# Optimization experiments

Hardware: AMD Instinct MI355X
Metric: run time of the kernel (lower is better)

Reference implementation:

```python
import jax, jax.numpy as jnp
import numpy as np

N_SUBKEYS = 256
D_KEY = 128
D_MODEL = 1024
TOP_K = 8


def setup_inputs() -> dict:
    key = jax.random.key(0)
    ks = jax.random.split(key, 7)
    B, T = 4, 2048
    x = jax.random.normal(ks[0], (B, T, D_MODEL), dtype=jnp.float32)
    keys_a = jax.random.normal(ks[1], (N_SUBKEYS, D_KEY), dtype=jnp.float32) * 0.02
    keys_b = jax.random.normal(ks[2], (N_SUBKEYS, D_KEY), dtype=jnp.float32) * 0.02
    values = jax.random.normal(ks[3], (N_SUBKEYS * N_SUBKEYS, D_MODEL), dtype=jnp.float32) * 0.01
    # nn.Linear(d_model, 2*d_key, bias=False): weight shape [2*d_key, d_model]
    Wq = jax.random.normal(ks[4], (2 * D_KEY, D_MODEL), dtype=jnp.float32) * (1.0 / np.sqrt(D_MODEL))
    gate_w = jax.random.normal(ks[5], (1, D_MODEL), dtype=jnp.float32) * (1.0 / np.sqrt(D_MODEL))
    gate_b = jnp.full((1,), -2.0, dtype=jnp.float32)
    return {"x": x, "keys_a": keys_a, "keys_b": keys_b, "values": values,
            "Wq": Wq, "gate_w": gate_w, "gate_b": gate_b}


def reference(x, keys_a, keys_b, values, Wq, gate_w, gate_b):
    B, T, D = x.shape
    tk = TOP_K
    q = jnp.einsum('btd,kd->btk', x, Wq)          # [B,T,2*d_key]
    qa, qb = jnp.split(q, 2, axis=-1)
    scores_a = jnp.einsum('btd,nd->btn', qa, keys_a)  # [B,T,n_subkeys]
    scores_b = jnp.einsum('btd,nd->btn', qb, keys_b)
    va, ia = jax.lax.top_k(scores_a, tk)          # [B,T,tk]
    vb, ib = jax.lax.top_k(scores_b, tk)
    # Cartesian combination of sub-key candidates -> tk*tk flat candidates
    flat_idx = (ia[..., :, None] * N_SUBKEYS + ib[..., None, :]).reshape(B, T, tk * tk)
    combined = (va[..., :, None] + vb[..., None, :]).reshape(B, T, tk * tk)
    fv, fi = jax.lax.top_k(combined, tk)          # [B,T,tk]
    final_idx = jnp.take_along_axis(flat_idx, fi, axis=-1)  # [B,T,tk]
    weights = jax.nn.softmax(fv, axis=-1)
    vals = values[final_idx]                      # [B,T,tk,D] gather from big table
    mem_out = jnp.einsum('btk,btkd->btd', weights, vals)
    g = jax.nn.sigmoid(jnp.einsum('btd,od->bto', x, gate_w) + gate_b)  # [B,T,1]
    return x + g * mem_out
```

## Files before the change

kernel.cpp:

```cpp
#include <hip/hip_runtime.h>
#include <math.h>

#define D_MODEL 1024
#define D_KEY 128
#define NSUB 256
#define NTOK 8192

typedef __attribute__((ext_vector_type(8))) short bf16x8;
typedef __attribute__((ext_vector_type(4))) float f32x4;

__device__ __forceinline__ unsigned short f2bf(float f) {
  union { float f; unsigned int u; } v; v.f = f;
  return (unsigned short)((v.u + 0x7fffu + ((v.u >> 16) & 1u)) >> 16);
}
__device__ __forceinline__ float bf2f(unsigned short u) {
  union { unsigned int u; float f; } v; v.u = ((unsigned int)u) << 16;
  return v.f;
}

__global__ __launch_bounds__(256) void k_prep(const float* __restrict__ Wq,
                                              const float* __restrict__ keys_a,
                                              const float* __restrict__ keys_b,
                                              unsigned short* __restrict__ Mt) {
  __shared__ float ks[4][128];
  const int tid = threadIdx.x;
  const int c0 = blockIdx.x * 4;
  const float* kk = (c0 < 256) ? keys_a : keys_b;
  const int rbase = c0 & 255;
  const int joff = (c0 < 256) ? 0 : 128;
  if (tid < 128) {
    const int r = tid >> 5, f = tid & 31;
    *(float4*)&ks[r][f * 4] = *(const float4*)&kk[(size_t)(rbase + r) * 128 + f * 4];
  }
  __syncthreads();
  const int d0 = tid * 4;
  float acc[4][4] = {};
  for (int j = 0; j < 128; j++) {
    const float4 wv = *(const float4*)&Wq[(size_t)(joff + j) * D_MODEL + d0];
#pragma unroll
    for (int r = 0; r < 4; r++) {
      const float kj = ks[r][j];
      acc[r][0] += wv.x * kj; acc[r][1] += wv.y * kj;
      acc[r][2] += wv.z * kj; acc[r][3] += wv.w * kj;
    }
  }
#pragma unroll
  for (int r = 0; r < 4; r++) {
    ushort4 o;
    o.x = f2bf(acc[r][0]); o.y = f2bf(acc[r][1]);
    o.z = f2bf(acc[r][2]); o.w = f2bf(acc[r][3]);
    *(ushort4*)&Mt[(size_t)(c0 + r) * D_MODEL + d0] = o;
  }
}

__global__ __launch_bounds__(256) void k_scores(const float* __restrict__ x,
                                                const unsigned short* __restrict__ Mt,
                                                unsigned short* __restrict__ scores) {
  __shared__ __align__(16) short Asd[64 * 32];
  __shared__ __align__(16) short Bsd[128 * 32];
  const int tid = threadIdx.x;
  const int t0 = blockIdx.y * 64;
  const int c0 = blockIdx.x * 128;
  const int arow = tid >> 2, aseg = tid & 3;
  const int brow = tid >> 1, bhalf = tid & 1;
  const float* xp = x + (size_t)(t0 + arow) * D_MODEL + aseg * 8;
  const unsigned short* mp = Mt + (size_t)(c0 + brow) * D_MODEL + bhalf * 16;
  const int l = tid & 63, w = tid >> 6;
  const int rw0 = (w & 1) * 32;
  const int cw0 = (w >> 1) * 64;
  const int fr = l & 15, q = l >> 4;

  f32x4 acc[2][4];
#pragma unroll
  for (int mi = 0; mi < 2; mi++)
#pragma unroll
    for (int ni = 0; ni < 4; ni++) acc[mi][ni] = (f32x4){0.f, 0.f, 0.f, 0.f};

  for (int kc = 0; kc < D_MODEL; kc += 32) {
    const float4 a0 = *(const float4*)(xp + kc);
    const float4 a1 = *(const float4*)(xp + kc + 4);
    bf16x8 pk;
    pk[0] = (short)f2bf(a0.x); pk[1] = (short)f2bf(a0.y);
    pk[2] = (short)f2bf(a0.z); pk[3] = (short)f2bf(a0.w);
    pk[4] = (short)f2bf(a1.x); pk[5] = (short)f2bf(a1.y);
    pk[6] = (short)f2bf(a1.z); pk[7] = (short)f2bf(a1.w);
    *(bf16x8*)&Asd[arow * 32 + aseg * 8] = pk;
    const uint4 b0 = *(const uint4*)(mp + kc);
    const uint4 b1 = *(const uint4*)(mp + kc + 8);
    *(uint4*)&Bsd[brow * 32 + bhalf * 16] = b0;
    *(uint4*)&Bsd[brow * 32 + bhalf * 16 + 8] = b1;
    __syncthreads();
    bf16x8 af[2], bfr[4];
#pragma unroll
    for (int mi = 0; mi < 2; mi++)
      af[mi] = *(const bf16x8*)&Asd[(rw0 + mi * 16 + fr) * 32 + q * 8];
#pragma unroll
    for (int ni = 0; ni < 4; ni++)
      bfr[ni] = *(const bf16x8*)&Bsd[(cw0 + ni * 16 + fr) * 32 + q * 8];
#pragma unroll
    for (int mi = 0; mi < 2; mi++)
#pragma unroll
      for (int ni = 0; ni < 4; ni++)
        acc[mi][ni] = __builtin_amdgcn_mfma_f32_16x16x32_bf16(af[mi], bfr[ni], acc[mi][ni], 0, 0, 0);
    __syncthreads();
  }
#pragma unroll
  for (int mi = 0; mi < 2; mi++)
#pragma unroll
    for (int ni = 0; ni < 4; ni++)
#pragma unroll
      for (int r = 0; r < 4; r++) {
        const int row = t0 + rw0 + mi * 16 + q * 4 + r;
        const int col = c0 + cw0 + ni * 16 + fr;
        scores[(size_t)row * 512 + col] = f2bf(acc[mi][ni][r]);
      }
}

__global__ __launch_bounds__(256) void k_topk(const float* __restrict__ x,
                                              const float* __restrict__ values,
                                              const float* __restrict__ gate_w,
                                              const float* __restrict__ gate_b,
                                              const unsigned short* __restrict__ scores,
                                              float* __restrict__ out) {
  const int tid = threadIdx.x;
  const int lane = tid & 63;
  const int wave = tid >> 6;
  const size_t t = (size_t)blockIdx.x * 4 + wave;

  const unsigned short* srow = scores + t * 512;
  const ushort4 ra = *(const ushort4*)&srow[lane * 4];
  const ushort4 rb = *(const ushort4*)&srow[256 + lane * 4];
  float sva[4] = {bf2f(ra.x), bf2f(ra.y), bf2f(ra.z), bf2f(ra.w)};
  float svb[4] = {bf2f(rb.x), bf2f(rb.y), bf2f(rb.z), bf2f(rb.w)};

  float tav[8], tbv[8];
  int tai[8], tbi[8];
#pragma unroll
  for (int sel = 0; sel < 8; sel++) {
    float bv = sva[0]; int bi = lane * 4;
#pragma unroll
    for (int c = 1; c < 4; c++)
      if (sva[c] > bv) { bv = sva[c]; bi = lane * 4 + c; }
#pragma unroll
    for (int off = 32; off >= 1; off >>= 1) {
      const float ov = __shfl_xor(bv, off);
      const int oi = __shfl_xor(bi, off);
      if (ov > bv || (ov == bv && oi < bi)) { bv = ov; bi = oi; }
    }
    tav[sel] = bv; tai[sel] = bi;
    if ((bi >> 2) == lane) sva[bi & 3] = -INFINITY;
  }
#pragma unroll
  for (int sel = 0; sel < 8; sel++) {
    float bv = svb[0]; int bi = lane * 4;
#pragma unroll
    for (int c = 1; c < 4; c++)
      if (svb[c] > bv) { bv = svb[c]; bi = lane * 4 + c; }
#pragma unroll
    for (int off = 32; off >= 1; off >>= 1) {
      const float ov = __shfl_xor(bv, off);
      const int oi = __shfl_xor(bi, off);
      if (ov > bv || (ov == bv && oi < bi)) { bv = ov; bi = oi; }
    }
    tbv[sel] = bv; tbi[sel] = bi;
    if ((bi >> 2) == lane) svb[bi & 3] = -INFINITY;
  }
  float cv = tav[lane >> 3] + tbv[lane & 7];
  float fv[8]; int fidx[8];
#pragma unroll
  for (int sel = 0; sel < 8; sel++) {
    float bv = cv; int bi = lane;
#pragma unroll
    for (int off = 32; off >= 1; off >>= 1) {
      const float ov = __shfl_xor(bv, off);
      const int oi = __shfl_xor(bi, off);
      if (ov > bv || (ov == bv && oi < bi)) { bv = ov; bi = oi; }
    }
    fv[sel] = bv;
    fidx[sel] = tai[bi >> 3] * NSUB + tbi[bi & 7];
    if (lane == bi) cv = -INFINITY;
  }
  float wgt[8];
  {
    float s = 0.f;
#pragma unroll
    for (int k = 0; k < 8; k++) { wgt[k] = __expf(fv[k] - fv[0]); s += wgt[k]; }
    const float inv = 1.0f / s;
#pragma unroll
    for (int k = 0; k < 8; k++) wgt[k] *= inv;
  }

  const size_t base = t * D_MODEL + lane * 16;
  float4 xv[4], gw[4];
#pragma unroll
  for (int u = 0; u < 4; u++) {
    xv[u] = *(const float4*)&x[base + u * 4];
    gw[u] = *(const float4*)&gate_w[lane * 16 + u * 4];
  }
  float gp = 0.f;
#pragma unroll
  for (int u = 0; u < 4; u++)
    gp += xv[u].x * gw[u].x + xv[u].y * gw[u].y + xv[u].z * gw[u].z + xv[u].w * gw[u].w;
#pragma unroll
  for (int off = 32; off >= 1; off >>= 1) gp += __shfl_xor(gp, off);
  const float g = 1.0f / (1.0f + __expf(-(gp + gate_b[0])));

  float4 facc[4] = {{0, 0, 0, 0}, {0, 0, 0, 0}, {0, 0, 0, 0}, {0, 0, 0, 0}};
#pragma unroll
  for (int k = 0; k < 8; k++) {
    const float wk = wgt[k];
    const float* vrow = values + (size_t)fidx[k] * D_MODEL + lane * 16;
#pragma unroll
    for (int u = 0; u < 4; u++) {
      const float4 v4 = *(const float4*)&vrow[u * 4];
      facc[u].x += wk * v4.x; facc[u].y += wk * v4.y;
      facc[u].z += wk * v4.z; facc[u].w += wk * v4.w;
    }
  }
#pragma unroll
  for (int u = 0; u < 4; u++) {
    float4 o;
    o.x = xv[u].x + g * facc[u].x; o.y = xv[u].y + g * facc[u].y;
    o.z = xv[u].z + g * facc[u].z; o.w = xv[u].w + g * facc[u].w;
    *(float4*)&out[base + u * 4] = o;
  }
}

extern "C" void kernel_launch(void* const* d_in, const int* in_sizes, int n_in,
                              void* d_out, int out_size, void* d_ws, size_t ws_size,
                              hipStream_t stream) {
  const float* x = (const float*)d_in[0];
  const float* keys_a = (const float*)d_in[1];
  const float* keys_b = (const float*)d_in[2];
  const float* values = (const float*)d_in[3];
  const float* Wq = (const float*)d_in[4];
  const float* gate_w = (const float*)d_in[5];
  const float* gate_b = (const float*)d_in[6];
  float* out = (float*)d_out;

  unsigned short* scores = (unsigned short*)d_ws;
  unsigned short* Mt = (unsigned short*)((char*)d_ws + (size_t)NTOK * 512 * 2);

  k_prep<<<128, 256, 0, stream>>>(Wq, keys_a, keys_b, Mt);
  k_scores<<<dim3(4, 128), 256, 0, stream>>>(x, Mt, scores);
  k_topk<<<NTOK / 4, 256, 0, stream>>>(x, values, gate_w, gate_b, scores, out);
}
```

Baseline: 515.2 us.

## Split top-k selection and value gather into separate kernels

The fused top-k plus gather kernel is split in two. A selection kernel writes the softmax weights and flat indices per token to workspace. A separate gather kernel then uses one 256-thread block per token, each thread loading one float4 per value row, with the gate dot product reduced across waves through shared memory. The aim is more parallelism and memory-level concurrency for the random gather of value rows, at the cost of an extra launch and a small round trip of indices and weights through global memory.

After: 464.1 us. 9.9% less time.

```diff
diff --git a/kernel.cpp b/kernel.cpp
--- a/kernel.cpp
+++ b/kernel.cpp
@@ -116,12 +116,9 @@
       }
 }
 
-__global__ __launch_bounds__(256) void k_topk(const float* __restrict__ x,
-                                              const float* __restrict__ values,
-                                              const float* __restrict__ gate_w,
-                                              const float* __restrict__ gate_b,
-                                              const unsigned short* __restrict__ scores,
-                                              float* __restrict__ out) {
+__global__ __launch_bounds__(256) void k_topk_sel(const unsigned short* __restrict__ scores,
+                                                  float* __restrict__ wout,
+                                                  int* __restrict__ iout) {
   const int tid = threadIdx.x;
   const int lane = tid & 63;
   const int wave = tid >> 6;
@@ -181,49 +178,60 @@
     if (lane == bi) cv = -INFINITY;
   }
   float wgt[8];
-  {
-    float s = 0.f;
-#pragma unroll
-    for (int k = 0; k < 8; k++) { wgt[k] = __expf(fv[k] - fv[0]); s += wgt[k]; }
-    const float inv = 1.0f / s;
-#pragma unroll
-    for (int k = 0; k < 8; k++) wgt[k] *= inv;
-  }
-
-  const size_t base = t * D_MODEL + lane * 16;
-  float4 xv[4], gw[4];
-#pragma unroll
-  for (int u = 0; u < 4; u++) {
-    xv[u] = *(const float4*)&x[base + u * 4];
-    gw[u] = *(const float4*)&gate_w[lane * 16 + u * 4];
-  }
-  float gp = 0.f;
-#pragma unroll
-  for (int u = 0; u < 4; u++)
-    gp += xv[u].x * gw[u].x + xv[u].y * gw[u].y + xv[u].z * gw[u].z + xv[u].w * gw[u].w;
+  float s = 0.f;
+#pragma unroll
+  for (int k = 0; k < 8; k++) { wgt[k] = __expf(fv[k] - fv[0]); s += wgt[k]; }
+  const float inv = 1.0f / s;
+#pragma unroll
+  for (int k = 0; k < 8; k++) wgt[k] *= inv;
+
+  if (lane == 0) {
+    *(float4*)&wout[t * 8] = make_float4(wgt[0], wgt[1], wgt[2], wgt[3]);
+    *(float4*)&wout[t * 8 + 4] = make_float4(wgt[4], wgt[5], wgt[6], wgt[7]);
+    *(int4*)&iout[t * 8] = make_int4(fidx[0], fidx[1], fidx[2], fidx[3]);
+    *(int4*)&iout[t * 8 + 4] = make_int4(fidx[4], fidx[5], fidx[6], fidx[7]);
+  }
+}
+
+__global__ __launch_bounds__(256) void k_gather(const float* __restrict__ x,
+                                                const float* __restrict__ values,
+                                                const float* __restrict__ gate_w,
+                                                const float* __restrict__ gate_b,
+                                                const float* __restrict__ win,
+                                                const int* __restrict__ iin,
+                                                float* __restrict__ out) {
+  __shared__ float swgt[8];
+  __shared__ int sidx[8];
+  __shared__ float gpart[4];
+  const int tid = threadIdx.x;
+  const int lane = tid & 63;
+  const int wave = tid >> 6;
+  const size_t t = blockIdx.x;
+
+  if (tid < 2) *(float4*)&swgt[tid * 4] = *(const float4*)&win[t * 8 + tid * 4];
+  else if (tid < 4) *(int4*)&sidx[(tid - 2) * 4] = *(const int4*)&iin[t * 8 + (tid - 2) * 4];
+
+  const float4 x4 = *(const float4*)&x[t * D_MODEL + tid * 4];
+  const float4 gw4 = *(const float4*)&gate_w[tid * 4];
+  float gp = x4.x * gw4.x + x4.y * gw4.y + x4.z * gw4.z + x4.w * gw4.w;
 #pragma unroll
   for (int off = 32; off >= 1; off >>= 1) gp += __shfl_xor(gp, off);
-  const float g = 1.0f / (1.0f + __expf(-(gp + gate_b[0])));
-
-  float4 facc[4] = {{0, 0, 0, 0}, {0, 0, 0, 0}, {0, 0, 0, 0}, {0, 0, 0, 0}};
+  if (lane == 0) gpart[wave] = gp;
+  __syncthreads();
+
+  const float g = 1.0f / (1.0f + __expf(-(gpart[0] + gpart[1] + gpart[2] + gpart[3] + gate_b[0])));
+  float4 acc = make_float4(0.f, 0.f, 0.f, 0.f);
 #pragma unroll
   for (int k = 0; k < 8; k++) {
-    const float wk = wgt[k];
-    const float* vrow = values + (size_t)fidx[k] * D_MODEL + lane * 16;
-#pragma unroll
-    for (int u = 0; u < 4; u++) {
-      const float4 v4 = *(const float4*)&vrow[u * 4];
-      facc[u].x += wk * v4.x; facc[u].y += wk * v4.y;
-      facc[u].z += wk * v4.z; facc[u].w += wk * v4.w;
-    }
-  }
-#pragma unroll
-  for (int u = 0; u < 4; u++) {
-    float4 o;
-    o.x = xv[u].x + g * facc[u].x; o.y = xv[u].y + g * facc[u].y;
-    o.z = xv[u].z + g * facc[u].z; o.w = xv[u].w + g * facc[u].w;
-    *(float4*)&out[base + u * 4] = o;
-  }
+    const float wk = swgt[k];
+    const float4 v4 = *(const float4*)&values[(size_t)sidx[k] * D_MODEL + tid * 4];
+    acc.x += wk * v4.x; acc.y += wk * v4.y;
+    acc.z += wk * v4.z; acc.w += wk * v4.w;
+  }
+  float4 o;
+  o.x = x4.x + g * acc.x; o.y = x4.y + g * acc.y;
+  o.z = x4.z + g * acc.z; o.w = x4.w + g * acc.w;
+  *(float4*)&out[t * D_MODEL + tid * 4] = o;
 }
 
 extern "C" void kernel_launch(void* const* d_in, const int* in_sizes, int n_in,
@@ -238,10 +246,14 @@
   const float* gate_b = (const float*)d_in[6];
   float* out = (float*)d_out;
 
-  unsigned short* scores = (unsigned short*)d_ws;
-  unsigned short* Mt = (unsigned short*)((char*)d_ws + (size_t)NTOK * 512 * 2);
+  char* ws = (char*)d_ws;
+  unsigned short* scores = (unsigned short*)ws;
+  unsigned short* Mt = (unsigned short*)(ws + (size_t)NTOK * 512 * 2);
+  float* wbuf = (float*)(ws + 9u * 1024 * 1024);
+  int* ibuf = (int*)(ws + 9u * 1024 * 1024 + 256 * 1024);
 
   k_prep<<<128, 256, 0, stream>>>(Wq, keys_a, keys_b, Mt);
   k_scores<<<dim3(4, 128), 256, 0, stream>>>(x, Mt, scores);
-  k_topk<<<NTOK / 4, 256, 0, stream>>>(x, values, gate_w, gate_b, scores, out);
-}
+  k_topk_sel<<<NTOK / 4, 256, 0, stream>>>(scores, wbuf, ibuf);
+  k_gather<<<NTOK, 256, 0, stream>>>(x, values, gate_w, gate_b, wbuf, ibuf, out);
+}
```
